# Kernel tuning notes

Measured on AMD Instinct MI355X. Metric: run time of the kernel, lower is better.

The kernel has to match this reference:

```python
import jax, jax.numpy as jnp
import numpy as np


def _lstm_layer(x_seq, w_ih, w_hh, b_ih, b_hh):
    # x_seq: [T, in], PyTorch gate order i, f, g, o
    H = w_hh.shape[1]
    h0 = jnp.zeros((H,), x_seq.dtype)

    def step(carry, x_t):
        h, c = carry
        gates = x_t @ w_ih.T + h @ w_hh.T + b_ih + b_hh  # [4H]
        i, f, g, o = jnp.split(gates, 4)
        i = jax.nn.sigmoid(i)
        f = jax.nn.sigmoid(f)
        g = jnp.tanh(g)
        o = jax.nn.sigmoid(o)
        c = f * c + i * g
        h = o * jnp.tanh(c)
        return (h, c), h

    _, hs = jax.lax.scan(step, (h0, h0), x_seq)
    return hs  # [T, H]


def setup_inputs() -> dict:
    key = jax.random.key(0)
    ks = jax.random.split(key, 12)
    B, T, n, H = 8, 128, 32, 128
    s = 1.0 / np.sqrt(H)

    def u(k, shape):
        return jax.random.uniform(k, shape, jnp.float32, -s, s)

    return {
        "x": jax.random.normal(ks[0], (B, T, n, n), jnp.float32),
        "w_ih0": u(ks[1], (4 * H, 1)),
        "w_hh0": u(ks[2], (4 * H, H)),
        "b_ih0": u(ks[3], (4 * H,)),
        "b_hh0": u(ks[4], (4 * H,)),
        "w_ih1": u(ks[5], (4 * H, H)),
        "w_hh1": u(ks[6], (4 * H, H)),
        "b_ih1": u(ks[7], (4 * H,)),
        "b_hh1": u(ks[8], (4 * H,)),
        "w_out": u(ks[9], (1, H)),
        "b_out": u(ks[10], (1,)),
    }


def reference(x, w_ih0, w_hh0, b_ih0, b_hh0, w_ih1, w_hh1, b_ih1, b_hh1, w_out, b_out):
    # x: [B, T, n, n]
    def rnn_forward(xi):  # xi: [T, n, n] -> out [T, 1]
        u = jnp.trace(xi, axis1=-2, axis2=-1)[:, None]  # [T, 1]
        h1 = _lstm_layer(u, w_ih0, w_hh0, b_ih0, b_hh0)
        h2 = _lstm_layer(h1, w_ih1, w_hh1, b_ih1, b_hh1)
        return h2 @ w_out.T + b_out  # [T, 1]

    jac = jax.vmap(jax.jacrev(rnn_forward))(x)  # [B, T, 1, T, n, n]
    d = jnp.diagonal(jac, axis1=1, axis2=3)      # [B, 1, n, n, T]
    # mirror torch: [:, 0] then transpose(2,3).transpose(1,2) -> [B, T, n, n]
    return jnp.transpose(d[:, 0], (0, 3, 1, 2))
```

## Files before the change

kernel.cpp:

```cpp
#include <hip/hip_runtime.h>
#include <math.h>

#define H    128
#define TT   128
#define CH   8
#define NCH  (TT / CH)

#define OFF_H1V   0
#define OFF_PARTS 262144
#define OFF_GPART 1310720
#define OFF_CNT   1441792

__device__ __forceinline__ float sigf(float x)       { return 1.0f / (1.0f + __expf(-x)); }
__device__ __forceinline__ float tanhf_fast(float x) { return 1.0f - 2.0f / (1.0f + __expf(2.0f * x)); }

__device__ __forceinline__ float quad_sum(float v) {
    int t = __builtin_amdgcn_update_dpp(0, __float_as_int(v), 0xB1, 0xF, 0xF, true);
    v += __int_as_float(t);
    t = __builtin_amdgcn_update_dpp(0, __float_as_int(v), 0x4E, 0xF, 0xF, true);
    v += __int_as_float(t);
    return v;
}

__device__ __forceinline__ void wait_ge(int* ptr, int val) {
    while (__hip_atomic_load(ptr, __ATOMIC_RELAXED, __HIP_MEMORY_SCOPE_AGENT) < val)
        __builtin_amdgcn_s_sleep(1);
    (void)__hip_atomic_load(ptr, __ATOMIC_ACQUIRE, __HIP_MEMORY_SCOPE_AGENT);
}

#define DECLW4(nm, src) \
    float4 _t_##nm = (src); \
    float nm##_x = _t_##nm.x, nm##_y = _t_##nm.y, nm##_z = _t_##nm.z, nm##_w = _t_##nm.w; \
    asm volatile("" : "+v"(nm##_x), "+v"(nm##_y), "+v"(nm##_z), "+v"(nm##_w));

#define LOADW_ALL(W) \
    const float4* wpa_ = (const float4*)((W) + (size_t)(rg)       * H + p * 32); \
    const float4* wpb_ = (const float4*)((W) + (size_t)(rg + 128) * H + p * 32); \
    const float4* wpc_ = (const float4*)((W) + (size_t)(rg + 256) * H + p * 32); \
    const float4* wpd_ = (const float4*)((W) + (size_t)(rg + 384) * H + p * 32); \
    DECLW4(wa0, wpa_[0]) DECLW4(wa1, wpa_[1]) DECLW4(wa2, wpa_[2]) DECLW4(wa3, wpa_[3]) \
    DECLW4(wa4, wpa_[4]) DECLW4(wa5, wpa_[5]) DECLW4(wa6, wpa_[6]) DECLW4(wa7, wpa_[7]) \
    DECLW4(wb0, wpb_[0]) DECLW4(wb1, wpb_[1]) DECLW4(wb2, wpb_[2]) DECLW4(wb3, wpb_[3]) \
    DECLW4(wb4, wpb_[4]) DECLW4(wb5, wpb_[5]) DECLW4(wb6, wpb_[6]) DECLW4(wb7, wpb_[7]) \
    DECLW4(wc0, wpc_[0]) DECLW4(wc1, wpc_[1]) DECLW4(wc2, wpc_[2]) DECLW4(wc3, wpc_[3]) \
    DECLW4(wc4, wpc_[4]) DECLW4(wc5, wpc_[5]) DECLW4(wc6, wpc_[6]) DECLW4(wc7, wpc_[7]) \
    DECLW4(wd0, wpd_[0]) DECLW4(wd1, wpd_[1]) DECLW4(wd2, wpd_[2]) DECLW4(wd3, wpd_[3]) \
    DECLW4(wd4, wpd_[4]) DECLW4(wd5, wpd_[5]) DECLW4(wd6, wpd_[6]) DECLW4(wd7, wpd_[7])

#define FMA1(nm, ov, acc) \
    acc = fmaf(nm##_x, ov.x, acc); acc = fmaf(nm##_y, ov.y, acc); \
    acc = fmaf(nm##_z, ov.z, acc); acc = fmaf(nm##_w, ov.w, acc);

#define DOTJ(j) FMA1(wa##j, hv##j, a0) FMA1(wb##j, hv##j, a1) FMA1(wc##j, hv##j, a2) FMA1(wd##j, hv##j, a3)

#define DOT_BODY(HBASE) \
    const float4* _hp4 = (const float4*)(HBASE); \
    float4 hv0=_hp4[0],hv1=_hp4[1],hv2=_hp4[2],hv3=_hp4[3], \
           hv4=_hp4[4],hv5=_hp4[5],hv6=_hp4[6],hv7=_hp4[7]; \
    float a0=0.f,a1=0.f,a2=0.f,a3=0.f; \
    DOTJ(0) DOTJ(1) DOTJ(2) DOTJ(3) DOTJ(4) DOTJ(5) DOTJ(6) DOTJ(7) \
    a0 = quad_sum(a0); a1 = quad_sum(a1); a2 = quad_sum(a2); a3 = quad_sum(a3);

__global__ __launch_bounds__(512, 1)
void pipe_kernel(const float* __restrict__ x,
                 const float* __restrict__ w_ih0,
                 const float* __restrict__ w_hh0,
                 const float* __restrict__ b_ih0,
                 const float* __restrict__ b_hh0,
                 const float* __restrict__ w_ih1,
                 const float* __restrict__ w_hh1,
                 const float* __restrict__ b_ih1,
                 const float* __restrict__ b_hh1,
                 const float* __restrict__ w_out,
                 float* __restrict__ ws) {
    const int role = blockIdx.x >> 3;
    const int b    = blockIdx.x & 7;
    const int r    = threadIdx.x;
    const int rg   = r >> 2, p = r & 3;
    const int wsl  = rg >> 5, wpos = rg & 31;

    int* cntA  = (int*)ws + OFF_CNT       + b * 32;
    int* cntB1 = (int*)ws + OFF_CNT + 256 + b * 32;
    int* cntB2 = (int*)ws + OFF_CNT + 512 + b * 32;
    float* h1v = ws + OFF_H1V + (size_t)b * TT * 256;

    __shared__ float hbuf[2][144];
    __shared__ float u_s[TT];
    __shared__ float scr[512];
    __shared__ float hb[CH * 144];

    if (role == 0) {
        LOADW_ALL(w_hh0)
        const float b0 = b_ih0[rg]       + b_hh0[rg];
        const float b1 = b_ih0[rg + 128] + b_hh0[rg + 128];
        const float b2 = b_ih0[rg + 256] + b_hh0[rg + 256];
        const float b3 = b_ih0[rg + 384] + b_hh0[rg + 384];
        const float wi0 = w_ih0[rg], wi1 = w_ih0[rg + 128];
        const float wi2 = w_ih0[rg + 256], wi3 = w_ih0[rg + 384];
        {
            const float* xb = x + (size_t)(b * TT + (r & 127)) * 1024;
            const int pq = r >> 7;
            float u = 0.f;
#pragma unroll
            for (int i = 0; i < 8; i++) u += xb[(pq * 8 + i) * 33];
            scr[r] = u;
        }
        if (r < 144) hbuf[0][r] = 0.f;
        __syncthreads();
        if (r < TT) u_s[r] = scr[r] + scr[r + 128] + scr[r + 256] + scr[r + 384];
        __syncthreads();

        float c1 = 0.f;
        for (int t = 0; t < TT; t++) {
            const float* hc = hbuf[t & 1];
            float* hx = hbuf[(t & 1) ^ 1];
            DOT_BODY(hc + p * 36)
            const float u = u_s[t];
            float z0 = a0 + fmaf(wi0, u, b0);
            float z1 = a1 + fmaf(wi1, u, b1);
            float z2 = a2 + fmaf(wi2, u, b2);
            float z3 = a3 + fmaf(wi3, u, b3);
            float gi = sigf(z0), gf = sigf(z1), gg = tanhf_fast(z2), go = sigf(z3);
            float di = gi * (1.f - gi) * wi0, df = gf * (1.f - gf) * wi1;
            float dg = (1.f - gg * gg) * wi2, dd = go * (1.f - go) * wi3;
            float dc = df * c1 + di * gg + gi * dg;
            c1 = gf * c1 + gi * gg;
            float th = tanhf_fast(c1);
            float hn = go * th;
            float vn = dd * th + go * (1.f - th * th) * dc;
            if (p == wsl) hx[p * 36 + wpos] = hn;
            if (p == 0) h1v[t * 256 + rg] = hn;
            if (p == 1) h1v[t * 256 + 128 + rg] = vn;
            __syncthreads();
            if ((t & (CH - 1)) == CH - 1 && r == 0)
                __hip_atomic_store(cntA, t + 1, __ATOMIC_RELEASE, __HIP_MEMORY_SCOPE_AGENT);
        }
    } else if (role == 1 || role == 2) {
        LOADW_ALL(w_ih1)
        int* myCnt = (role == 2) ? cntB2 : cntB1;
        const float* hsrc = h1v + ((role == 2) ? 128 : 0);
        float* pbase = ws + OFF_PARTS + (size_t)b * TT * 1024 + ((role == 2) ? 512 : 0);
        for (int c = 0; c < NCH; c++) {
            if (r == 0) wait_ge(cntA, (c + 1) * CH);
            __syncthreads();
            if (r < 256) {
                int tl = r >> 5, k4 = r & 31, s = k4 >> 3, j = k4 & 7;
                float4 v = *(const float4*)(hsrc + (size_t)(c * CH + tl) * 256 + k4 * 4);
                *(float4*)&hb[(tl * 4 + s) * 36 + j * 4] = v;
            }
            __syncthreads();
#pragma unroll
            for (int tl = 0; tl < CH; tl++) {
                DOT_BODY(hb + (tl * 4 + p) * 36)
                float sel = (p == 0) ? a0 : (p == 1) ? a1 : (p == 2) ? a2 : a3;
                pbase[(size_t)(c * CH + tl) * 1024 + r] = sel;
            }
            __syncthreads();
            if (r == 0)
                __hip_atomic_store(myCnt, (c + 1) * CH, __ATOMIC_RELEASE, __HIP_MEMORY_SCOPE_AGENT);
        }
    } else {
        LOADW_ALL(w_hh1)
        const float b0 = b_ih1[rg]       + b_hh1[rg];
        const float b1 = b_ih1[rg + 128] + b_hh1[rg + 128];
        const float b2 = b_ih1[rg + 256] + b_hh1[rg + 256];
        const float b3 = b_ih1[rg + 384] + b_hh1[rg + 384];
        const float wo = w_out[rg];
        if (r < 144) hbuf[0][r] = 0.f;
        __syncthreads();
        const float* parts = ws + OFF_PARTS + (size_t)b * TT * 1024;
        float* gpart = ws + OFF_GPART + (size_t)b * TT * 128;
        float c2 = 0.f;
        for (int c = 0; c < NCH; c++) {
            if (r == 0) { wait_ge(cntB1, (c + 1) * CH); wait_ge(cntB2, (c + 1) * CH); }
            __syncthreads();
            float4 zf[CH], af[CH];
#pragma unroll
            for (int tl = 0; tl < CH; tl++) {
                zf[tl] = *(const float4*)(parts + (size_t)(c * CH + tl) * 1024 + rg * 4);
                af[tl] = *(const float4*)(parts + (size_t)(c * CH + tl) * 1024 + 512 + rg * 4);
            }
#pragma unroll
            for (int tl = 0; tl < CH; tl++) {
                const int t = c * CH + tl;
                const float* hc = hbuf[t & 1];
                float* hx = hbuf[(t & 1) ^ 1];
                DOT_BODY(hc + p * 36)
                float z0 = a0 + b0 + zf[tl].x;
                float z1 = a1 + b1 + zf[tl].y;
                float z2 = a2 + b2 + zf[tl].z;
                float z3 = a3 + b3 + zf[tl].w;
                float gi = sigf(z0), gf = sigf(z1), gg = tanhf_fast(z2), go = sigf(z3);
                float di = gi * (1.f - gi) * af[tl].x, df = gf * (1.f - gf) * af[tl].y;
                float dg = (1.f - gg * gg) * af[tl].z, dd = go * (1.f - go) * af[tl].w;
                float dc = df * c2 + di * gg + gi * dg;
                c2 = gf * c2 + gi * gg;
                float th = tanhf_fast(c2);
                if (p == wsl) hx[p * 36 + wpos] = go * th;
                float dh2 = dd * th + go * (1.f - th * th) * dc;
                if (p == 0) gpart[t * 128 + rg] = wo * dh2;
                __syncthreads();
            }
        }
    }
}

__global__ __launch_bounds__(256)
void fill_kernel(const float* __restrict__ gpart, float4* __restrict__ out4) {
    const int bt = blockIdx.x;
    const int r  = threadIdx.x;
    __shared__ float red[129];
    if (r < 128) red[r] = gpart[(size_t)bt * 128 + r];
    __syncthreads();
    if (r < 64) {
        float v = red[r] + red[r + 64];
#pragma unroll
        for (int s = 32; s > 0; s >>= 1) v += __shfl_down(v, s, 64);
        if (r == 0) red[128] = v;
    }
    __syncthreads();
    const float g = red[128];
    const int m  = r * 4;
    const int i  = m >> 5, j0 = m & 31;
    float4 v;
    v.x = (j0     == i) ? g : 0.f;
    v.y = (j0 + 1 == i) ? g : 0.f;
    v.z = (j0 + 2 == i) ? g : 0.f;
    v.w = (j0 + 3 == i) ? g : 0.f;
    out4[(size_t)bt * 256 + r] = v;
}

extern "C" void kernel_launch(void* const* d_in, const int* in_sizes, int n_in,
                              void* d_out, int out_size, void* d_ws, size_t ws_size,
                              hipStream_t stream) {
    const float* x     = (const float*)d_in[0];
    const float* w_ih0 = (const float*)d_in[1];
    const float* w_hh0 = (const float*)d_in[2];
    const float* b_ih0 = (const float*)d_in[3];
    const float* b_hh0 = (const float*)d_in[4];
    const float* w_ih1 = (const float*)d_in[5];
    const float* w_hh1 = (const float*)d_in[6];
    const float* b_ih1 = (const float*)d_in[7];
    const float* b_hh1 = (const float*)d_in[8];
    const float* w_out = (const float*)d_in[9];

    float* ws = (float*)d_ws;

    pipe_kernel<<<dim3(32), dim3(512), 0, stream>>>(x, w_ih0, w_hh0, b_ih0, b_hh0,
                                                    w_ih1, w_hh1, b_ih1, b_hh1, w_out,
                                                    ws);
    fill_kernel<<<dim3(1024), dim3(256), 0, stream>>>(ws + OFF_GPART, (float4*)d_out);
}
```

Before: 240.3 us.

## Process two batch elements per block to reuse register-held weights

Each pipeline block now handles two batch elements at once, interleaving two independent recurrences over the same register-resident weight rows. The grid shrinks from 32 to 16 blocks, and the dot-product macro computes both sequences' gate sums in one pass. This is meant to hide the latency of the serial per-step chain by giving each step twice the independent work, and to halve weight loading per block. The cost is more live registers and longer steps, which could lengthen the critical path per timestep. The stage-3 block also loses its per-chunk prefetch of partial sums and now loads them inside each step.

```diff
diff --git a/kernel.cpp b/kernel.cpp
--- a/kernel.cpp
+++ b/kernel.cpp
@@ -51,15 +51,23 @@
     acc = fmaf(nm##_x, ov.x, acc); acc = fmaf(nm##_y, ov.y, acc); \
     acc = fmaf(nm##_z, ov.z, acc); acc = fmaf(nm##_w, ov.w, acc);
 
-#define DOTJ(j) FMA1(wa##j, hv##j, a0) FMA1(wb##j, hv##j, a1) FMA1(wc##j, hv##j, a2) FMA1(wd##j, hv##j, a3)
-
-#define DOT_BODY(HBASE) \
-    const float4* _hp4 = (const float4*)(HBASE); \
-    float4 hv0=_hp4[0],hv1=_hp4[1],hv2=_hp4[2],hv3=_hp4[3], \
-           hv4=_hp4[4],hv5=_hp4[5],hv6=_hp4[6],hv7=_hp4[7]; \
-    float a0=0.f,a1=0.f,a2=0.f,a3=0.f; \
-    DOTJ(0) DOTJ(1) DOTJ(2) DOTJ(3) DOTJ(4) DOTJ(5) DOTJ(6) DOTJ(7) \
-    a0 = quad_sum(a0); a1 = quad_sum(a1); a2 = quad_sum(a2); a3 = quad_sum(a3);
+#define DOTJ2(j) \
+    FMA1(wa##j, hv##j, a0) FMA1(wa##j, gv##j, e0) \
+    FMA1(wb##j, hv##j, a1) FMA1(wb##j, gv##j, e1) \
+    FMA1(wc##j, hv##j, a2) FMA1(wc##j, gv##j, e2) \
+    FMA1(wd##j, hv##j, a3) FMA1(wd##j, gv##j, e3)
+
+#define DOT2_BODY(H0, H1) \
+    const float4* _q0 = (const float4*)(H0); \
+    const float4* _q1 = (const float4*)(H1); \
+    float4 hv0=_q0[0],hv1=_q0[1],hv2=_q0[2],hv3=_q0[3], \
+           hv4=_q0[4],hv5=_q0[5],hv6=_q0[6],hv7=_q0[7]; \
+    float4 gv0=_q1[0],gv1=_q1[1],gv2=_q1[2],gv3=_q1[3], \
+           gv4=_q1[4],gv5=_q1[5],gv6=_q1[6],gv7=_q1[7]; \
+    float a0=0.f,a1=0.f,a2=0.f,a3=0.f,e0=0.f,e1=0.f,e2=0.f,e3=0.f; \
+    DOTJ2(0) DOTJ2(1) DOTJ2(2) DOTJ2(3) DOTJ2(4) DOTJ2(5) DOTJ2(6) DOTJ2(7) \
+    a0 = quad_sum(a0); e0 = quad_sum(e0); a1 = quad_sum(a1); e1 = quad_sum(e1); \
+    a2 = quad_sum(a2); e2 = quad_sum(e2); a3 = quad_sum(a3); e3 = quad_sum(e3);
 
 __global__ __launch_bounds__(512, 1)
 void pipe_kernel(const float* __restrict__ x,
@@ -73,21 +81,25 @@
                  const float* __restrict__ b_hh1,
                  const float* __restrict__ w_out,
                  float* __restrict__ ws) {
-    const int role = blockIdx.x >> 3;
-    const int b    = blockIdx.x & 7;
+    const int role = blockIdx.x >> 2;
+    const int bp   = blockIdx.x & 3;
+    const int b0i  = bp * 2, b1i = bp * 2 + 1;
     const int r    = threadIdx.x;
     const int rg   = r >> 2, p = r & 3;
     const int wsl  = rg >> 5, wpos = rg & 31;
 
-    int* cntA  = (int*)ws + OFF_CNT       + b * 32;
-    int* cntB1 = (int*)ws + OFF_CNT + 256 + b * 32;
-    int* cntB2 = (int*)ws + OFF_CNT + 512 + b * 32;
-    float* h1v = ws + OFF_H1V + (size_t)b * TT * 256;
-
-    __shared__ float hbuf[2][144];
-    __shared__ float u_s[TT];
+    int* cntA  = (int*)ws + OFF_CNT       + bp * 32;
+    int* cntB1 = (int*)ws + OFF_CNT + 256 + bp * 32;
+    int* cntB2 = (int*)ws + OFF_CNT + 512 + bp * 32;
+    float* h1v0 = ws + OFF_H1V + (size_t)b0i * TT * 256;
+    float* h1v1 = ws + OFF_H1V + (size_t)b1i * TT * 256;
+
+    __shared__ float hbufA[2][144];
+    __shared__ float hbufB[2][144];
+    __shared__ float u_s[2][TT];
     __shared__ float scr[512];
-    __shared__ float hb[CH * 144];
+    __shared__ float hb0[CH * 144];
+    __shared__ float hb1[CH * 144];
 
     if (role == 0) {
         LOADW_ALL(w_hh0)
@@ -97,40 +109,53 @@
         const float b3 = b_ih0[rg + 384] + b_hh0[rg + 384];
         const float wi0 = w_ih0[rg], wi1 = w_ih0[rg + 128];
         const float wi2 = w_ih0[rg + 256], wi3 = w_ih0[rg + 384];
-        {
-            const float* xb = x + (size_t)(b * TT + (r & 127)) * 1024;
+        for (int q = 0; q < 2; q++) {
+            const int bb = bp * 2 + q;
+            const float* xb = x + (size_t)(bb * TT + (r & 127)) * 1024;
             const int pq = r >> 7;
             float u = 0.f;
 #pragma unroll
             for (int i = 0; i < 8; i++) u += xb[(pq * 8 + i) * 33];
             scr[r] = u;
-        }
-        if (r < 144) hbuf[0][r] = 0.f;
+            __syncthreads();
+            if (r < TT) u_s[q][r] = scr[r] + scr[r + 128] + scr[r + 256] + scr[r + 384];
+            __syncthreads();
+        }
+        if (r < 144) { hbufA[0][r] = 0.f; hbufB[0][r] = 0.f; }
         __syncthreads();
-        if (r < TT) u_s[r] = scr[r] + scr[r + 128] + scr[r + 256] + scr[r + 384];
-        __syncthreads();
-
-        float c1 = 0.f;
+
+        float c1a = 0.f, c1b = 0.f;
         for (int t = 0; t < TT; t++) {
-            const float* hc = hbuf[t & 1];
-            float* hx = hbuf[(t & 1) ^ 1];
-            DOT_BODY(hc + p * 36)
-            const float u = u_s[t];
-            float z0 = a0 + fmaf(wi0, u, b0);
-            float z1 = a1 + fmaf(wi1, u, b1);
-            float z2 = a2 + fmaf(wi2, u, b2);
-            float z3 = a3 + fmaf(wi3, u, b3);
+            const float* hcA = hbufA[t & 1];
+            float* hxA = hbufA[(t & 1) ^ 1];
+            const float* hcB = hbufB[t & 1];
+            float* hxB = hbufB[(t & 1) ^ 1];
+            DOT2_BODY(hcA + p * 36, hcB + p * 36)
+            const float u0 = u_s[0][t], u1 = u_s[1][t];
+            float z0 = a0 + fmaf(wi0, u0, b0), z1 = a1 + fmaf(wi1, u0, b1);
+            float z2 = a2 + fmaf(wi2, u0, b2), z3 = a3 + fmaf(wi3, u0, b3);
             float gi = sigf(z0), gf = sigf(z1), gg = tanhf_fast(z2), go = sigf(z3);
             float di = gi * (1.f - gi) * wi0, df = gf * (1.f - gf) * wi1;
             float dg = (1.f - gg * gg) * wi2, dd = go * (1.f - go) * wi3;
-            float dc = df * c1 + di * gg + gi * dg;
-            c1 = gf * c1 + gi * gg;
-            float th = tanhf_fast(c1);
-            float hn = go * th;
-            float vn = dd * th + go * (1.f - th * th) * dc;
-            if (p == wsl) hx[p * 36 + wpos] = hn;
-            if (p == 0) h1v[t * 256 + rg] = hn;
-            if (p == 1) h1v[t * 256 + 128 + rg] = vn;
+            float dc = df * c1a + di * gg + gi * dg;
+            c1a = gf * c1a + gi * gg;
+            float th = tanhf_fast(c1a);
+            float hn0 = go * th;
+            float vn0 = dd * th + go * (1.f - th * th) * dc;
+            float y0 = e0 + fmaf(wi0, u1, b0), y1 = e1 + fmaf(wi1, u1, b1);
+            float y2 = e2 + fmaf(wi2, u1, b2), y3 = e3 + fmaf(wi3, u1, b3);
+            float gi1 = sigf(y0), gf1 = sigf(y1), gg1 = tanhf_fast(y2), go1 = sigf(y3);
+            float di1 = gi1 * (1.f - gi1) * wi0, df1 = gf1 * (1.f - gf1) * wi1;
+            float dg1 = (1.f - gg1 * gg1) * wi2, dd1 = go1 * (1.f - go1) * wi3;
+            float dc1 = df1 * c1b + di1 * gg1 + gi1 * dg1;
+            c1b = gf1 * c1b + gi1 * gg1;
+            float th1 = tanhf_fast(c1b);
+            float hn1 = go1 * th1;
+            float vn1 = dd1 * th1 + go1 * (1.f - th1 * th1) * dc1;
+
+            if (p == wsl) { hxA[p * 36 + wpos] = hn0; hxB[p * 36 + wpos] = hn1; }
+            if (p == 0) { h1v0[t * 256 + rg] = hn0; h1v1[t * 256 + rg] = hn1; }
+            if (p == 1) { h1v0[t * 256 + 128 + rg] = vn0; h1v1[t * 256 + 128 + rg] = vn1; }
             __syncthreads();
             if ((t & (CH - 1)) == CH - 1 && r == 0)
                 __hip_atomic_store(cntA, t + 1, __ATOMIC_RELEASE, __HIP_MEMORY_SCOPE_AGENT);
@@ -138,22 +163,30 @@
     } else if (role == 1 || role == 2) {
         LOADW_ALL(w_ih1)
         int* myCnt = (role == 2) ? cntB2 : cntB1;
-        const float* hsrc = h1v + ((role == 2) ? 128 : 0);
-        float* pbase = ws + OFF_PARTS + (size_t)b * TT * 1024 + ((role == 2) ? 512 : 0);
+        const int off = (role == 2) ? 128 : 0;
+        const float* hsrc0 = h1v0 + off;
+        const float* hsrc1 = h1v1 + off;
+        float* pb0 = ws + OFF_PARTS + (size_t)b0i * TT * 1024 + ((role == 2) ? 512 : 0);
+        float* pb1 = ws + OFF_PARTS + (size_t)b1i * TT * 1024 + ((role == 2) ? 512 : 0);
         for (int c = 0; c < NCH; c++) {
             if (r == 0) wait_ge(cntA, (c + 1) * CH);
             __syncthreads();
-            if (r < 256) {
-                int tl = r >> 5, k4 = r & 31, s = k4 >> 3, j = k4 & 7;
-                float4 v = *(const float4*)(hsrc + (size_t)(c * CH + tl) * 256 + k4 * 4);
-                *(float4*)&hb[(tl * 4 + s) * 36 + j * 4] = v;
+            {
+                const int q = r >> 8, rr = r & 255;
+                const float* hs = q ? hsrc1 : hsrc0;
+                float* hbq = q ? hb1 : hb0;
+                int tl = rr >> 5, k4 = rr & 31, s = k4 >> 3, j = k4 & 7;
+                float4 v = *(const float4*)(hs + (size_t)(c * CH + tl) * 256 + k4 * 4);
+                *(float4*)&hbq[(tl * 4 + s) * 36 + j * 4] = v;
             }
             __syncthreads();
 #pragma unroll
             for (int tl = 0; tl < CH; tl++) {
-                DOT_BODY(hb + (tl * 4 + p) * 36)
-                float sel = (p == 0) ? a0 : (p == 1) ? a1 : (p == 2) ? a2 : a3;
-                pbase[(size_t)(c * CH + tl) * 1024 + r] = sel;
+                DOT2_BODY(hb0 + (tl * 4 + p) * 36, hb1 + (tl * 4 + p) * 36)
+                float s0 = (p == 0) ? a0 : (p == 1) ? a1 : (p == 2) ? a2 : a3;
+                float s1 = (p == 0) ? e0 : (p == 1) ? e1 : (p == 2) ? e2 : e3;
+                pb0[(size_t)(c * CH + tl) * 1024 + r] = s0;
+                pb1[(size_t)(c * CH + tl) * 1024 + r] = s1;
             }
             __syncthreads();
             if (r == 0)
@@ -166,39 +199,49 @@
         const float b2 = b_ih1[rg + 256] + b_hh1[rg + 256];
         const float b3 = b_ih1[rg + 384] + b_hh1[rg + 384];
         const float wo = w_out[rg];
-        if (r < 144) hbuf[0][r] = 0.f;
+        if (r < 144) { hbufA[0][r] = 0.f; hbufB[0][r] = 0.f; }
         __syncthreads();
-        const float* parts = ws + OFF_PARTS + (size_t)b * TT * 1024;
-        float* gpart = ws + OFF_GPART + (size_t)b * TT * 128;
-        float c2 = 0.f;
+        const float* pt0 = ws + OFF_PARTS + (size_t)b0i * TT * 1024;
+        const float* pt1 = ws + OFF_PARTS + (size_t)b1i * TT * 1024;
+        float* gp0 = ws + OFF_GPART + (size_t)b0i * TT * 128;
+        float* gp1 = ws + OFF_GPART + (size_t)b1i * TT * 128;
+        float c2a = 0.f, c2b = 0.f;
         for (int c = 0; c < NCH; c++) {
             if (r == 0) { wait_ge(cntB1, (c + 1) * CH); wait_ge(cntB2, (c + 1) * CH); }
             __syncthreads();
-            float4 zf[CH], af[CH];
-#pragma unroll
-            for (int tl = 0; tl < CH; tl++) {
-                zf[tl] = *(const float4*)(parts + (size_t)(c * CH + tl) * 1024 + rg * 4);
-                af[tl] = *(const float4*)(parts + (size_t)(c * CH + tl) * 1024 + 512 + rg * 4);
-            }
 #pragma unroll
             for (int tl = 0; tl < CH; tl++) {
                 const int t = c * CH + tl;
-                const float* hc = hbuf[t & 1];
-                float* hx = hbuf[(t & 1) ^ 1];
-                DOT_BODY(hc + p * 36)
-                float z0 = a0 + b0 + zf[tl].x;
-                float z1 = a1 + b1 + zf[tl].y;
-                float z2 = a2 + b2 + zf[tl].z;
-                float z3 = a3 + b3 + zf[tl].w;
+                float4 zfa = *(const float4*)(pt0 + (size_t)t * 1024 + rg * 4);
+                float4 afa = *(const float4*)(pt0 + (size_t)t * 1024 + 512 + rg * 4);
+                float4 zfb = *(const float4*)(pt1 + (size_t)t * 1024 + rg * 4);
+                float4 afb = *(const float4*)(pt1 + (size_t)t * 1024 + 512 + rg * 4);
+                const float* hcA = hbufA[t & 1];
+                float* hxA = hbufA[(t & 1) ^ 1];
+                const float* hcB = hbufB[t & 1];
+                float* hxB = hbufB[(t & 1) ^ 1];
+                DOT2_BODY(hcA + p * 36, hcB + p * 36)
+                float z0 = a0 + b0 + zfa.x, z1 = a1 + b1 + zfa.y;
+                float z2 = a2 + b2 + zfa.z, z3 = a3 + b3 + zfa.w;
                 float gi = sigf(z0), gf = sigf(z1), gg = tanhf_fast(z2), go = sigf(z3);
-                float di = gi * (1.f - gi) * af[tl].x, df = gf * (1.f - gf) * af[tl].y;
-                float dg = (1.f - gg * gg) * af[tl].z, dd = go * (1.f - go) * af[tl].w;
-                float dc = df * c2 + di * gg + gi * dg;
-                c2 = gf * c2 + gi * gg;
-                float th = tanhf_fast(c2);
-                if (p == wsl) hx[p * 36 + wpos] = go * th;
-                float dh2 = dd * th + go * (1.f - th * th) * dc;
-                if (p == 0) gpart[t * 128 + rg] = wo * dh2;
+                float di = gi * (1.f - gi) * afa.x, df = gf * (1.f - gf) * afa.y;
+                float dg = (1.f - gg * gg) * afa.z, dd = go * (1.f - go) * afa.w;
+                float dc = df * c2a + di * gg + gi * dg;
+                c2a = gf * c2a + gi * gg;
+                float th = tanhf_fast(c2a);
+                float dh0 = dd * th + go * (1.f - th * th) * dc;
+                float y0 = e0 + b0 + zfb.x, y1 = e1 + b1 + zfb.y;
+                float y2 = e2 + b2 + zfb.z, y3 = e3 + b3 + zfb.w;
+                float gi1 = sigf(y0), gf1 = sigf(y1), gg1 = tanhf_fast(y2), go1 = sigf(y3);
+                float di1 = gi1 * (1.f - gi1) * afb.x, df1 = gf1 * (1.f - gf1) * afb.y;
+                float dg1 = (1.f - gg1 * gg1) * afb.z, dd1 = go1 * (1.f - go1) * afb.w;
+                float dc1 = df1 * c2b + di1 * gg1 + gi1 * dg1;
+                c2b = gf1 * c2b + gi1 * gg1;
+                float th1 = tanhf_fast(c2b);
+                float dh1 = dd1 * th1 + go1 * (1.f - th1 * th1) * dc1;
+
+                if (p == wsl) { hxA[p * 36 + wpos] = go * th; hxB[p * 36 + wpos] = go1 * th1; }
+                if (p == 0) { gp0[t * 128 + rg] = wo * dh0; gp1[t * 128 + rg] = wo * dh1; }
                 __syncthreads();
             }
         }
@@ -246,7 +289,7 @@
 
     float* ws = (float*)d_ws;
 
-    pipe_kernel<<<dim3(32), dim3(512), 0, stream>>>(x, w_ih0, w_hh0, b_ih0, b_hh0,
+    pipe_kernel<<<dim3(16), dim3(512), 0, stream>>>(x, w_ih0, w_hh0, b_ih0, b_hh0,
                                                     w_ih1, w_hh1, b_ih1, b_hh1, w_out,
                                                     ws);
     fill_kernel<<<dim3(1024), dim3(256), 0, stream>>>(ws + OFF_GPART, (float4*)d_out);
```

New measurement: 366.2 us. +52.4%, slower.

## Split each gate-row dot product across eight lanes with 1024-thread blocks

Applied to the files above, without the earlier changes.

Blocks grow from 512 to 1024 threads, and each group of 4 gate rows is now handled by 8 lanes instead of 4. Each lane holds a 16-wide slice of the weights in registers instead of 32, which halves the serial FMA chain per recurrence step. The partial sums are combined with an extra cross-lane shuffle, and the shared h buffers are re-padded to a stride of 20. This aims to cut per-step latency on the sequential LSTM critical path, at the cost of an extra shuffle, more threads taking part in each barrier, and per-step global loads for the layer-2 preactivations in place of chunk-level prefetch.

```diff
diff --git a/kernel.cpp b/kernel.cpp
--- a/kernel.cpp
+++ b/kernel.cpp
@@ -14,11 +14,12 @@
 __device__ __forceinline__ float sigf(float x)       { return 1.0f / (1.0f + __expf(-x)); }
 __device__ __forceinline__ float tanhf_fast(float x) { return 1.0f - 2.0f / (1.0f + __expf(2.0f * x)); }
 
-__device__ __forceinline__ float quad_sum(float v) {
+__device__ __forceinline__ float oct_sum(float v) {
     int t = __builtin_amdgcn_update_dpp(0, __float_as_int(v), 0xB1, 0xF, 0xF, true);
     v += __int_as_float(t);
     t = __builtin_amdgcn_update_dpp(0, __float_as_int(v), 0x4E, 0xF, 0xF, true);
     v += __int_as_float(t);
+    v += __shfl_xor(v, 4, 64);
     return v;
 }
 
@@ -33,35 +34,34 @@
     float nm##_x = _t_##nm.x, nm##_y = _t_##nm.y, nm##_z = _t_##nm.z, nm##_w = _t_##nm.w; \
     asm volatile("" : "+v"(nm##_x), "+v"(nm##_y), "+v"(nm##_z), "+v"(nm##_w));
 
-#define LOADW_ALL(W) \
-    const float4* wpa_ = (const float4*)((W) + (size_t)(rg)       * H + p * 32); \
-    const float4* wpb_ = (const float4*)((W) + (size_t)(rg + 128) * H + p * 32); \
-    const float4* wpc_ = (const float4*)((W) + (size_t)(rg + 256) * H + p * 32); \
-    const float4* wpd_ = (const float4*)((W) + (size_t)(rg + 384) * H + p * 32); \
+#define LOADW8(W) \
+    const float4* wpa_ = (const float4*)((W) + (size_t)(rg)       * H + p * 16); \
+    const float4* wpb_ = (const float4*)((W) + (size_t)(rg + 128) * H + p * 16); \
+    const float4* wpc_ = (const float4*)((W) + (size_t)(rg + 256) * H + p * 16); \
+    const float4* wpd_ = (const float4*)((W) + (size_t)(rg + 384) * H + p * 16); \
     DECLW4(wa0, wpa_[0]) DECLW4(wa1, wpa_[1]) DECLW4(wa2, wpa_[2]) DECLW4(wa3, wpa_[3]) \
-    DECLW4(wa4, wpa_[4]) DECLW4(wa5, wpa_[5]) DECLW4(wa6, wpa_[6]) DECLW4(wa7, wpa_[7]) \
     DECLW4(wb0, wpb_[0]) DECLW4(wb1, wpb_[1]) DECLW4(wb2, wpb_[2]) DECLW4(wb3, wpb_[3]) \
-    DECLW4(wb4, wpb_[4]) DECLW4(wb5, wpb_[5]) DECLW4(wb6, wpb_[6]) DECLW4(wb7, wpb_[7]) \
     DECLW4(wc0, wpc_[0]) DECLW4(wc1, wpc_[1]) DECLW4(wc2, wpc_[2]) DECLW4(wc3, wpc_[3]) \
-    DECLW4(wc4, wpc_[4]) DECLW4(wc5, wpc_[5]) DECLW4(wc6, wpc_[6]) DECLW4(wc7, wpc_[7]) \
-    DECLW4(wd0, wpd_[0]) DECLW4(wd1, wpd_[1]) DECLW4(wd2, wpd_[2]) DECLW4(wd3, wpd_[3]) \
-    DECLW4(wd4, wpd_[4]) DECLW4(wd5, wpd_[5]) DECLW4(wd6, wpd_[6]) DECLW4(wd7, wpd_[7])
+    DECLW4(wd0, wpd_[0]) DECLW4(wd1, wpd_[1]) DECLW4(wd2, wpd_[2]) DECLW4(wd3, wpd_[3])
 
 #define FMA1(nm, ov, acc) \
     acc = fmaf(nm##_x, ov.x, acc); acc = fmaf(nm##_y, ov.y, acc); \
     acc = fmaf(nm##_z, ov.z, acc); acc = fmaf(nm##_w, ov.w, acc);
 
-#define DOTJ(j) FMA1(wa##j, hv##j, a0) FMA1(wb##j, hv##j, a1) FMA1(wc##j, hv##j, a2) FMA1(wd##j, hv##j, a3)
-
-#define DOT_BODY(HBASE) \
-    const float4* _hp4 = (const float4*)(HBASE); \
-    float4 hv0=_hp4[0],hv1=_hp4[1],hv2=_hp4[2],hv3=_hp4[3], \
-           hv4=_hp4[4],hv5=_hp4[5],hv6=_hp4[6],hv7=_hp4[7]; \
-    float a0=0.f,a1=0.f,a2=0.f,a3=0.f; \
-    DOTJ(0) DOTJ(1) DOTJ(2) DOTJ(3) DOTJ(4) DOTJ(5) DOTJ(6) DOTJ(7) \
-    a0 = quad_sum(a0); a1 = quad_sum(a1); a2 = quad_sum(a2); a3 = quad_sum(a3);
-
-__global__ __launch_bounds__(512, 1)
+#define DOT8_BODY(HB) \
+    const float4* _hp4 = (const float4*)(HB); \
+    float4 hv0=_hp4[0], hv1=_hp4[1], hv2=_hp4[2], hv3=_hp4[3]; \
+    float a0=0.f, a1=0.f, a2=0.f, a3=0.f; \
+    FMA1(wa0, hv0, a0) FMA1(wb0, hv0, a1) FMA1(wc0, hv0, a2) FMA1(wd0, hv0, a3) \
+    FMA1(wa1, hv1, a0) FMA1(wb1, hv1, a1) FMA1(wc1, hv1, a2) FMA1(wd1, hv1, a3) \
+    FMA1(wa2, hv2, a0) FMA1(wb2, hv2, a1) FMA1(wc2, hv2, a2) FMA1(wd2, hv2, a3) \
+    FMA1(wa3, hv3, a0) FMA1(wb3, hv3, a1) FMA1(wc3, hv3, a2) FMA1(wd3, hv3, a3) \
+    a0 = oct_sum(a0); a1 = oct_sum(a1); a2 = oct_sum(a2); a3 = oct_sum(a3);
+
+#define HSTRIDE 20
+#define HBUFSZ  160
+
+__global__ __launch_bounds__(1024)
 void pipe_kernel(const float* __restrict__ x,
                  const float* __restrict__ w_ih0,
                  const float* __restrict__ w_hh0,
@@ -76,21 +76,23 @@
     const int role = blockIdx.x >> 3;
     const int b    = blockIdx.x & 7;
     const int r    = threadIdx.x;
-    const int rg   = r >> 2, p = r & 3;
-    const int wsl  = rg >> 5, wpos = rg & 31;
+    const int rg   = r >> 3;
+    const int p    = r & 7;
+    const int wsl  = rg >> 4;
+    const int wpos = rg & 15;
 
     int* cntA  = (int*)ws + OFF_CNT       + b * 32;
     int* cntB1 = (int*)ws + OFF_CNT + 256 + b * 32;
     int* cntB2 = (int*)ws + OFF_CNT + 512 + b * 32;
     float* h1v = ws + OFF_H1V + (size_t)b * TT * 256;
 
-    __shared__ float hbuf[2][144];
+    __shared__ float hbuf[2][HBUFSZ];
     __shared__ float u_s[TT];
-    __shared__ float scr[512];
-    __shared__ float hb[CH * 144];
+    __shared__ float scr[1024];
+    __shared__ float hb[CH * HBUFSZ];
 
     if (role == 0) {
-        LOADW_ALL(w_hh0)
+        LOADW8(w_hh0)
         const float b0 = b_ih0[rg]       + b_hh0[rg];
         const float b1 = b_ih0[rg + 128] + b_hh0[rg + 128];
         const float b2 = b_ih0[rg + 256] + b_hh0[rg + 256];
@@ -102,19 +104,24 @@
             const int pq = r >> 7;
             float u = 0.f;
 #pragma unroll
-            for (int i = 0; i < 8; i++) u += xb[(pq * 8 + i) * 33];
+            for (int i = 0; i < 4; i++) u += xb[(pq * 4 + i) * 33];
             scr[r] = u;
         }
-        if (r < 144) hbuf[0][r] = 0.f;
+        if (r < HBUFSZ) hbuf[0][r] = 0.f;
         __syncthreads();
-        if (r < TT) u_s[r] = scr[r] + scr[r + 128] + scr[r + 256] + scr[r + 384];
+        if (r < TT) {
+            float u = 0.f;
+#pragma unroll
+            for (int q = 0; q < 8; q++) u += scr[r + q * 128];
+            u_s[r] = u;
+        }
         __syncthreads();
 
         float c1 = 0.f;
         for (int t = 0; t < TT; t++) {
             const float* hc = hbuf[t & 1];
             float* hx = hbuf[(t & 1) ^ 1];
-            DOT_BODY(hc + p * 36)
+            DOT8_BODY(hc + p * HSTRIDE)
             const float u = u_s[t];
             float z0 = a0 + fmaf(wi0, u, b0);
             float z1 = a1 + fmaf(wi1, u, b1);
@@ -128,7 +135,7 @@
             float th = tanhf_fast(c1);
             float hn = go * th;
             float vn = dd * th + go * (1.f - th * th) * dc;
-            if (p == wsl) hx[p * 36 + wpos] = hn;
+            if (p == wsl) hx[wsl * HSTRIDE + wpos] = hn;
             if (p == 0) h1v[t * 256 + rg] = hn;
             if (p == 1) h1v[t * 256 + 128 + rg] = vn;
             __syncthreads();
@@ -136,7 +143,7 @@
                 __hip_atomic_store(cntA, t + 1, __ATOMIC_RELEASE, __HIP_MEMORY_SCOPE_AGENT);
         }
     } else if (role == 1 || role == 2) {
-        LOADW_ALL(w_ih1)
+        LOADW8(w_ih1)
         int* myCnt = (role == 2) ? cntB2 : cntB1;
         const float* hsrc = h1v + ((role == 2) ? 128 : 0);
         float* pbase = ws + OFF_PARTS + (size_t)b * TT * 1024 + ((role == 2) ? 512 : 0);
@@ -144,29 +151,31 @@
             if (r == 0) wait_ge(cntA, (c + 1) * CH);
             __syncthreads();
             if (r < 256) {
-                int tl = r >> 5, k4 = r & 31, s = k4 >> 3, j = k4 & 7;
+                int tl = r >> 5, k4 = r & 31, s = k4 >> 2, j = k4 & 3;
                 float4 v = *(const float4*)(hsrc + (size_t)(c * CH + tl) * 256 + k4 * 4);
-                *(float4*)&hb[(tl * 4 + s) * 36 + j * 4] = v;
+                *(float4*)&hb[tl * HBUFSZ + s * HSTRIDE + j * 4] = v;
             }
             __syncthreads();
 #pragma unroll
             for (int tl = 0; tl < CH; tl++) {
-                DOT_BODY(hb + (tl * 4 + p) * 36)
-                float sel = (p == 0) ? a0 : (p == 1) ? a1 : (p == 2) ? a2 : a3;
-                pbase[(size_t)(c * CH + tl) * 1024 + r] = sel;
+                DOT8_BODY(hb + tl * HBUFSZ + p * HSTRIDE)
+                if (p < 4) {
+                    float sel = (p == 0) ? a0 : (p == 1) ? a1 : (p == 2) ? a2 : a3;
+                    pbase[(size_t)(c * CH + tl) * 1024 + rg * 4 + p] = sel;
+                }
             }
             __syncthreads();
             if (r == 0)
                 __hip_atomic_store(myCnt, (c + 1) * CH, __ATOMIC_RELEASE, __HIP_MEMORY_SCOPE_AGENT);
         }
     } else {
-        LOADW_ALL(w_hh1)
+        LOADW8(w_hh1)
         const float b0 = b_ih1[rg]       + b_hh1[rg];
         const float b1 = b_ih1[rg + 128] + b_hh1[rg + 128];
         const float b2 = b_ih1[rg + 256] + b_hh1[rg + 256];
         const float b3 = b_ih1[rg + 384] + b_hh1[rg + 384];
         const float wo = w_out[rg];
-        if (r < 144) hbuf[0][r] = 0.f;
+        if (r < HBUFSZ) hbuf[0][r] = 0.f;
         __syncthreads();
         const float* parts = ws + OFF_PARTS + (size_t)b * TT * 1024;
         float* gpart = ws + OFF_GPART + (size_t)b * TT * 128;
@@ -174,29 +183,25 @@
         for (int c = 0; c < NCH; c++) {
             if (r == 0) { wait_ge(cntB1, (c + 1) * CH); wait_ge(cntB2, (c + 1) * CH); }
             __syncthreads();
-            float4 zf[CH], af[CH];
-#pragma unroll
-            for (int tl = 0; tl < CH; tl++) {
-                zf[tl] = *(const float4*)(parts + (size_t)(c * CH + tl) * 1024 + rg * 4);
-                af[tl] = *(const float4*)(parts + (size_t)(c * CH + tl) * 1024 + 512 + rg * 4);
-            }
 #pragma unroll
             for (int tl = 0; tl < CH; tl++) {
                 const int t = c * CH + tl;
+                float4 zf = *(const float4*)(parts + (size_t)t * 1024 + rg * 4);
+                float4 af = *(const float4*)(parts + (size_t)t * 1024 + 512 + rg * 4);
                 const float* hc = hbuf[t & 1];
                 float* hx = hbuf[(t & 1) ^ 1];
-                DOT_BODY(hc + p * 36)
-                float z0 = a0 + b0 + zf[tl].x;
-                float z1 = a1 + b1 + zf[tl].y;
-                float z2 = a2 + b2 + zf[tl].z;
-                float z3 = a3 + b3 + zf[tl].w;
+                DOT8_BODY(hc + p * HSTRIDE)
+                float z0 = a0 + b0 + zf.x;
+                float z1 = a1 + b1 + zf.y;
+                float z2 = a2 + b2 + zf.z;
+                float z3 = a3 + b3 + zf.w;
                 float gi = sigf(z0), gf = sigf(z1), gg = tanhf_fast(z2), go = sigf(z3);
-                float di = gi * (1.f - gi) * af[tl].x, df = gf * (1.f - gf) * af[tl].y;
-                float dg = (1.f - gg * gg) * af[tl].z, dd = go * (1.f - go) * af[tl].w;
+                float di = gi * (1.f - gi) * af.x, df = gf * (1.f - gf) * af.y;
+                float dg = (1.f - gg * gg) * af.z, dd = go * (1.f - go) * af.w;
                 float dc = df * c2 + di * gg + gi * dg;
                 c2 = gf * c2 + gi * gg;
                 float th = tanhf_fast(c2);
-                if (p == wsl) hx[p * 36 + wpos] = go * th;
+                if (p == wsl) hx[wsl * HSTRIDE + wpos] = go * th;
                 float dh2 = dd * th + go * (1.f - th * th) * dc;
                 if (p == 0) gpart[t * 128 + rg] = wo * dh2;
                 __syncthreads();
@@ -246,8 +251,8 @@
 
     float* ws = (float*)d_ws;
 
-    pipe_kernel<<<dim3(32), dim3(512), 0, stream>>>(x, w_ih0, w_hh0, b_ih0, b_hh0,
-                                                    w_ih1, w_hh1, b_ih1, b_hh1, w_out,
-                                                    ws);
+    pipe_kernel<<<dim3(32), dim3(1024), 0, stream>>>(x, w_ih0, w_hh0, b_ih0, b_hh0,
+                                                     w_ih1, w_hh1, b_ih1, b_hh1, w_out,
+                                                     ws);
     fill_kernel<<<dim3(1024), dim3(256), 0, stream>>>(ws + OFF_GPART, (float4*)d_out);
 }
```

After: 287.5 us. +19.7%, slower.

## Split LSTM weights between registers and LDS and fuse output fill into pipeline

Applied to the files above, without the earlier changes.

Each recurrent and input-projection block now keeps half of its weight slice in VGPRs and stages the other half in a padded LDS array that is read every step, which lowers register pressure. The separate fill kernel is removed. Its work becomes a fifth role of the pipelined kernel: it waits on a new per-chunk counter from the layer-2 role and writes the diagonal output as chunks finish. This removes a second launch and overlaps the output writes with the recurrence. In exchange, the latency-bound serial loop now carries extra LDS reads per step, and the layer-2 role loads its partial sums per step instead of prefetching a whole chunk.

```diff
diff --git a/kernel.cpp b/kernel.cpp
--- a/kernel.cpp
+++ b/kernel.cpp
@@ -10,6 +10,8 @@
 #define OFF_PARTS 262144
 #define OFF_GPART 1310720
 #define OFF_CNT   1441792
+
+#define WSTRIDE 68
 
 __device__ __forceinline__ float sigf(float x)       { return 1.0f / (1.0f + __expf(-x)); }
 __device__ __forceinline__ float tanhf_fast(float x) { return 1.0f - 2.0f / (1.0f + __expf(2.0f * x)); }
@@ -33,32 +35,49 @@
     float nm##_x = _t_##nm.x, nm##_y = _t_##nm.y, nm##_z = _t_##nm.z, nm##_w = _t_##nm.w; \
     asm volatile("" : "+v"(nm##_x), "+v"(nm##_y), "+v"(nm##_z), "+v"(nm##_w));
 
-#define LOADW_ALL(W) \
+#define LOADW_V(W) \
     const float4* wpa_ = (const float4*)((W) + (size_t)(rg)       * H + p * 32); \
     const float4* wpb_ = (const float4*)((W) + (size_t)(rg + 128) * H + p * 32); \
     const float4* wpc_ = (const float4*)((W) + (size_t)(rg + 256) * H + p * 32); \
     const float4* wpd_ = (const float4*)((W) + (size_t)(rg + 384) * H + p * 32); \
     DECLW4(wa0, wpa_[0]) DECLW4(wa1, wpa_[1]) DECLW4(wa2, wpa_[2]) DECLW4(wa3, wpa_[3]) \
-    DECLW4(wa4, wpa_[4]) DECLW4(wa5, wpa_[5]) DECLW4(wa6, wpa_[6]) DECLW4(wa7, wpa_[7]) \
     DECLW4(wb0, wpb_[0]) DECLW4(wb1, wpb_[1]) DECLW4(wb2, wpb_[2]) DECLW4(wb3, wpb_[3]) \
-    DECLW4(wb4, wpb_[4]) DECLW4(wb5, wpb_[5]) DECLW4(wb6, wpb_[6]) DECLW4(wb7, wpb_[7]) \
     DECLW4(wc0, wpc_[0]) DECLW4(wc1, wpc_[1]) DECLW4(wc2, wpc_[2]) DECLW4(wc3, wpc_[3]) \
-    DECLW4(wc4, wpc_[4]) DECLW4(wc5, wpc_[5]) DECLW4(wc6, wpc_[6]) DECLW4(wc7, wpc_[7]) \
-    DECLW4(wd0, wpd_[0]) DECLW4(wd1, wpd_[1]) DECLW4(wd2, wpd_[2]) DECLW4(wd3, wpd_[3]) \
-    DECLW4(wd4, wpd_[4]) DECLW4(wd5, wpd_[5]) DECLW4(wd6, wpd_[6]) DECLW4(wd7, wpd_[7])
+    DECLW4(wd0, wpd_[0]) DECLW4(wd1, wpd_[1]) DECLW4(wd2, wpd_[2]) DECLW4(wd3, wpd_[3])
+
+#define STAGE_WLDS(W) { \
+    float* dst = wlds + (size_t)r * WSTRIDE; \
+    _Pragma("unroll") \
+    for (int g = 0; g < 4; g++) { \
+        const float4* src = (const float4*)((W) + (size_t)(rg + 128 * g) * H + p * 32 + 16); \
+        _Pragma("unroll") \
+        for (int j = 0; j < 4; j++) *(float4*)(dst + (g * 4 + j) * 4) = src[j]; \
+    } }
 
 #define FMA1(nm, ov, acc) \
     acc = fmaf(nm##_x, ov.x, acc); acc = fmaf(nm##_y, ov.y, acc); \
     acc = fmaf(nm##_z, ov.z, acc); acc = fmaf(nm##_w, ov.w, acc);
 
-#define DOTJ(j) FMA1(wa##j, hv##j, a0) FMA1(wb##j, hv##j, a1) FMA1(wc##j, hv##j, a2) FMA1(wd##j, hv##j, a3)
-
-#define DOT_BODY(HBASE) \
+#define FMA4L(wv, hv, acc) \
+    acc = fmaf(wv.x, hv.x, acc); acc = fmaf(wv.y, hv.y, acc); \
+    acc = fmaf(wv.z, hv.z, acc); acc = fmaf(wv.w, hv.w, acc);
+
+#define DOT_HYB(HBASE) \
     const float4* _hp4 = (const float4*)(HBASE); \
+    const float4* _wl  = (const float4*)(wlds + (size_t)r * WSTRIDE); \
     float4 hv0=_hp4[0],hv1=_hp4[1],hv2=_hp4[2],hv3=_hp4[3], \
            hv4=_hp4[4],hv5=_hp4[5],hv6=_hp4[6],hv7=_hp4[7]; \
+    float4 l0=_wl[0],l1=_wl[1],l2=_wl[2],l3=_wl[3],l4=_wl[4],l5=_wl[5],l6=_wl[6],l7=_wl[7], \
+           l8=_wl[8],l9=_wl[9],l10=_wl[10],l11=_wl[11],l12=_wl[12],l13=_wl[13],l14=_wl[14],l15=_wl[15]; \
     float a0=0.f,a1=0.f,a2=0.f,a3=0.f; \
-    DOTJ(0) DOTJ(1) DOTJ(2) DOTJ(3) DOTJ(4) DOTJ(5) DOTJ(6) DOTJ(7) \
+    FMA1(wa0,hv0,a0) FMA1(wb0,hv0,a1) FMA1(wc0,hv0,a2) FMA1(wd0,hv0,a3) \
+    FMA1(wa1,hv1,a0) FMA1(wb1,hv1,a1) FMA1(wc1,hv1,a2) FMA1(wd1,hv1,a3) \
+    FMA1(wa2,hv2,a0) FMA1(wb2,hv2,a1) FMA1(wc2,hv2,a2) FMA1(wd2,hv2,a3) \
+    FMA1(wa3,hv3,a0) FMA1(wb3,hv3,a1) FMA1(wc3,hv3,a2) FMA1(wd3,hv3,a3) \
+    FMA4L(l0,hv4,a0)  FMA4L(l4,hv4,a1)  FMA4L(l8,hv4,a2)  FMA4L(l12,hv4,a3) \
+    FMA4L(l1,hv5,a0)  FMA4L(l5,hv5,a1)  FMA4L(l9,hv5,a2)  FMA4L(l13,hv5,a3) \
+    FMA4L(l2,hv6,a0)  FMA4L(l6,hv6,a1)  FMA4L(l10,hv6,a2) FMA4L(l14,hv6,a3) \
+    FMA4L(l3,hv7,a0)  FMA4L(l7,hv7,a1)  FMA4L(l11,hv7,a2) FMA4L(l15,hv7,a3) \
     a0 = quad_sum(a0); a1 = quad_sum(a1); a2 = quad_sum(a2); a3 = quad_sum(a3);
 
 __global__ __launch_bounds__(512, 1)
@@ -72,7 +91,8 @@
                  const float* __restrict__ b_ih1,
                  const float* __restrict__ b_hh1,
                  const float* __restrict__ w_out,
-                 float* __restrict__ ws) {
+                 float* __restrict__ ws,
+                 float4* __restrict__ out4) {
     const int role = blockIdx.x >> 3;
     const int b    = blockIdx.x & 7;
     const int r    = threadIdx.x;
@@ -82,15 +102,18 @@
     int* cntA  = (int*)ws + OFF_CNT       + b * 32;
     int* cntB1 = (int*)ws + OFF_CNT + 256 + b * 32;
     int* cntB2 = (int*)ws + OFF_CNT + 512 + b * 32;
+    int* cntC  = (int*)ws + OFF_CNT + 768 + b * 32;
     float* h1v = ws + OFF_H1V + (size_t)b * TT * 256;
 
+    __shared__ float wlds[512 * WSTRIDE];
     __shared__ float hbuf[2][144];
     __shared__ float u_s[TT];
     __shared__ float scr[512];
     __shared__ float hb[CH * 144];
 
     if (role == 0) {
-        LOADW_ALL(w_hh0)
+        LOADW_V(w_hh0)
+        STAGE_WLDS(w_hh0)
         const float b0 = b_ih0[rg]       + b_hh0[rg];
         const float b1 = b_ih0[rg + 128] + b_hh0[rg + 128];
         const float b2 = b_ih0[rg + 256] + b_hh0[rg + 256];
@@ -114,7 +137,7 @@
         for (int t = 0; t < TT; t++) {
             const float* hc = hbuf[t & 1];
             float* hx = hbuf[(t & 1) ^ 1];
-            DOT_BODY(hc + p * 36)
+            DOT_HYB(hc + p * 36)
             const float u = u_s[t];
             float z0 = a0 + fmaf(wi0, u, b0);
             float z1 = a1 + fmaf(wi1, u, b1);
@@ -136,7 +159,8 @@
                 __hip_atomic_store(cntA, t + 1, __ATOMIC_RELEASE, __HIP_MEMORY_SCOPE_AGENT);
         }
     } else if (role == 1 || role == 2) {
-        LOADW_ALL(w_ih1)
+        LOADW_V(w_ih1)
+        STAGE_WLDS(w_ih1)
         int* myCnt = (role == 2) ? cntB2 : cntB1;
         const float* hsrc = h1v + ((role == 2) ? 128 : 0);
         float* pbase = ws + OFF_PARTS + (size_t)b * TT * 1024 + ((role == 2) ? 512 : 0);
@@ -151,7 +175,7 @@
             __syncthreads();
 #pragma unroll
             for (int tl = 0; tl < CH; tl++) {
-                DOT_BODY(hb + (tl * 4 + p) * 36)
+                DOT_HYB(hb + (tl * 4 + p) * 36)
                 float sel = (p == 0) ? a0 : (p == 1) ? a1 : (p == 2) ? a2 : a3;
                 pbase[(size_t)(c * CH + tl) * 1024 + r] = sel;
             }
@@ -159,8 +183,9 @@
             if (r == 0)
                 __hip_atomic_store(myCnt, (c + 1) * CH, __ATOMIC_RELEASE, __HIP_MEMORY_SCOPE_AGENT);
         }
-    } else {
-        LOADW_ALL(w_hh1)
+    } else if (role == 3) {
+        LOADW_V(w_hh1)
+        STAGE_WLDS(w_hh1)
         const float b0 = b_ih1[rg]       + b_hh1[rg];
         const float b1 = b_ih1[rg + 128] + b_hh1[rg + 128];
         const float b2 = b_ih1[rg + 256] + b_hh1[rg + 256];
@@ -174,25 +199,21 @@
         for (int c = 0; c < NCH; c++) {
             if (r == 0) { wait_ge(cntB1, (c + 1) * CH); wait_ge(cntB2, (c + 1) * CH); }
             __syncthreads();
-            float4 zf[CH], af[CH];
-#pragma unroll
-            for (int tl = 0; tl < CH; tl++) {
-                zf[tl] = *(const float4*)(parts + (size_t)(c * CH + tl) * 1024 + rg * 4);
-                af[tl] = *(const float4*)(parts + (size_t)(c * CH + tl) * 1024 + 512 + rg * 4);
-            }
 #pragma unroll
             for (int tl = 0; tl < CH; tl++) {
                 const int t = c * CH + tl;
+                float4 zf = *(const float4*)(parts + (size_t)t * 1024 + rg * 4);
+                float4 af = *(const float4*)(parts + (size_t)t * 1024 + 512 + rg * 4);
                 const float* hc = hbuf[t & 1];
                 float* hx = hbuf[(t & 1) ^ 1];
-                DOT_BODY(hc + p * 36)
-                float z0 = a0 + b0 + zf[tl].x;
-                float z1 = a1 + b1 + zf[tl].y;
-                float z2 = a2 + b2 + zf[tl].z;
-                float z3 = a3 + b3 + zf[tl].w;
+                DOT_HYB(hc + p * 36)
+                float z0 = a0 + b0 + zf.x;
+                float z1 = a1 + b1 + zf.y;
+                float z2 = a2 + b2 + zf.z;
+                float z3 = a3 + b3 + zf.w;
                 float gi = sigf(z0), gf = sigf(z1), gg = tanhf_fast(z2), go = sigf(z3);
-                float di = gi * (1.f - gi) * af[tl].x, df = gf * (1.f - gf) * af[tl].y;
-                float dg = (1.f - gg * gg) * af[tl].z, dd = go * (1.f - go) * af[tl].w;
+                float di = gi * (1.f - gi) * af.x, df = gf * (1.f - gf) * af.y;
+                float dg = (1.f - gg * gg) * af.z, dd = go * (1.f - go) * af.w;
                 float dc = df * c2 + di * gg + gi * dg;
                 c2 = gf * c2 + gi * gg;
                 float th = tanhf_fast(c2);
@@ -201,33 +222,36 @@
                 if (p == 0) gpart[t * 128 + rg] = wo * dh2;
                 __syncthreads();
             }
+            if (r == 0)
+                __hip_atomic_store(cntC, (c + 1) * CH, __ATOMIC_RELEASE, __HIP_MEMORY_SCOPE_AGENT);
+        }
+    } else {
+        const float* gpart = ws + OFF_GPART + (size_t)b * TT * 128;
+        const int tloc = r >> 6;
+        const int lane = r & 63;
+        for (int c = 0; c < NCH; c++) {
+            if (r == 0) wait_ge(cntC, (c + 1) * CH);
+            __syncthreads();
+            const int t = c * CH + tloc;
+            float v = gpart[(size_t)t * 128 + lane] + gpart[(size_t)t * 128 + 64 + lane];
+#pragma unroll
+            for (int s = 32; s > 0; s >>= 1) v += __shfl_xor(v, s, 64);
+            const float g = v;
+            float4* ob = out4 + ((size_t)(b * TT) + t) * 256;
+#pragma unroll
+            for (int k = 0; k < 4; k++) {
+                const int m  = lane * 4 + k;
+                const int e0 = m * 4;
+                const int i  = (e0 >> 5) & 31, j0 = e0 & 31;
+                float4 o;
+                o.x = (j0     == i) ? g : 0.f;
+                o.y = (j0 + 1 == i) ? g : 0.f;
+                o.z = (j0 + 2 == i) ? g : 0.f;
+                o.w = (j0 + 3 == i) ? g : 0.f;
+                ob[m] = o;
+            }
         }
     }
-}
-
-__global__ __launch_bounds__(256)
-void fill_kernel(const float* __restrict__ gpart, float4* __restrict__ out4) {
-    const int bt = blockIdx.x;
-    const int r  = threadIdx.x;
-    __shared__ float red[129];
-    if (r < 128) red[r] = gpart[(size_t)bt * 128 + r];
-    __syncthreads();
-    if (r < 64) {
-        float v = red[r] + red[r + 64];
-#pragma unroll
-        for (int s = 32; s > 0; s >>= 1) v += __shfl_down(v, s, 64);
-        if (r == 0) red[128] = v;
-    }
-    __syncthreads();
-    const float g = red[128];
-    const int m  = r * 4;
-    const int i  = m >> 5, j0 = m & 31;
-    float4 v;
-    v.x = (j0     == i) ? g : 0.f;
-    v.y = (j0 + 1 == i) ? g : 0.f;
-    v.z = (j0 + 2 == i) ? g : 0.f;
-    v.w = (j0 + 3 == i) ? g : 0.f;
-    out4[(size_t)bt * 256 + r] = v;
 }
 
 extern "C" void kernel_launch(void* const* d_in, const int* in_sizes, int n_in,
@@ -246,8 +270,7 @@
 
     float* ws = (float*)d_ws;
 
-    pipe_kernel<<<dim3(32), dim3(512), 0, stream>>>(x, w_ih0, w_hh0, b_ih0, b_hh0,
+    pipe_kernel<<<dim3(40), dim3(512), 0, stream>>>(x, w_ih0, w_hh0, b_ih0, b_hh0,
                                                     w_ih1, w_hh1, b_ih1, b_hh1, w_out,
-                                                    ws);
-    fill_kernel<<<dim3(1024), dim3(256), 0, stream>>>(ws + OFF_GPART, (float4*)d_out);
-}
+                                                    ws, (float4*)d_out);
+}
```

Result: no change. 242.7 us (+1.0%).
